# Kernel tuning notes

Measured on AMD Instinct MI355X. Metric: run time of the kernel, lower is better.

## Reference

```python
import jax, jax.numpy as jnp
import numpy as np

MAX_N_LATENT = 8
EOS_THRESHOLD = 0.7
EOS_PATTERN_LEN = 3
COS_SIM_THRESHOLD = 0.3
EOS_SOFT_THRESHOLD = 0.5
CONTEXT_WINDOW = 2
EPS = 1e-8


def setup_inputs() -> dict:
    key = jax.random.key(0)
    k = jax.random.split(key, 8)
    B, S, D = 8, 4096, 1024
    s = 0.02
    latent_states = jax.random.normal(k[0], (B, S, D), dtype=jnp.float32)
    binary_mask = jax.random.randint(k[1], (B, S, 1), 0, 2).astype(jnp.int32)
    proj_w = jax.random.normal(k[2], (D, D), dtype=jnp.float32) * s
    proj_b = jax.random.normal(k[3], (D,), dtype=jnp.float32) * s
    eos_w1 = jax.random.normal(k[4], (D, D // 2), dtype=jnp.float32) * s
    eos_b1 = jax.random.normal(k[5], (D // 2,), dtype=jnp.float32) * s
    eos_w2 = jax.random.normal(k[6], (D // 2, 1), dtype=jnp.float32) * s
    eos_b2 = jax.random.normal(k[7], (1,), dtype=jnp.float32) * s
    return {"latent_states": latent_states, "binary_mask": binary_mask,
            "proj_w": proj_w, "proj_b": proj_b,
            "eos_w1": eos_w1, "eos_b1": eos_b1,
            "eos_w2": eos_w2, "eos_b2": eos_b2}


def reference(latent_states, binary_mask, proj_w, proj_b, eos_w1, eos_b1, eos_w2, eos_b2):
    B, S, D = latent_states.shape

    # ---- EOS scores (computed under no_grad in the original) ----
    h = jax.nn.relu(jnp.einsum('bsd,df->bsf', latent_states, eos_w1) + eos_b1)
    eos_scores = jax.nn.sigmoid(jnp.einsum('bsf,fo->bso', h, eos_w2) + eos_b2)[..., 0]
    eos_scores = jax.lax.stop_gradient(eos_scores)  # [B, S]

    # ---- segment ids: a boundary (mask==1) at i closes the patch that includes i ----
    m = binary_mask[..., 0].astype(jnp.int32)                 # [B, S]
    seg = jnp.cumsum(m, axis=1) - m                           # exclusive cumsum => patch id per token
    valid = (seg < MAX_N_LATENT).astype(latent_states.dtype)  # drop patches beyond MAX_N_LATENT (p[:max_patches])
    onehot = jax.nn.one_hot(jnp.clip(seg, 0, MAX_N_LATENT - 1), MAX_N_LATENT,
                            dtype=latent_states.dtype) * valid[..., None]  # [B, S, P]
    sums = jnp.einsum('bsp,bsd->bpd', onehot, latent_states)  # segmented sum
    counts = onehot.sum(axis=1)                               # [B, P]
    pooled = sums / jnp.maximum(counts, 1.0)[..., None]       # mean pooling; empty patches -> 0 (proj adds bias, as in torch)
    patches = jnp.einsum('bpd,do->bpo', pooled, proj_w) + proj_b  # [B, MAX_N_LATENT, output_dim]

    # ---- EOS bounds ----
    mthr = eos_scores > EOS_THRESHOLD
    run = mthr
    for t in range(1, EOS_PATTERN_LEN):                       # consecutive_eos_count >= EOS_PATTERN_LEN
        run = run & jnp.pad(mthr[:, :-t], ((0, 0), (t, 0)))
    a = latent_states[:, 1:-1]                                # prev state at i-1, for i >= 2
    b = latent_states[:, 2:]                                  # current state at i
    cos = (a * b).sum(-1) / (jnp.maximum(jnp.linalg.norm(a, axis=-1), EPS)
                             * jnp.maximum(jnp.linalg.norm(b, axis=-1), EPS))
    cos_rule = jnp.pad((cos < COS_SIM_THRESHOLD) & (eos_scores[:, 2:] > EOS_SOFT_THRESHOLD),
                       ((0, 0), (2, 0)))
    eos_any = run | cos_rule                                  # [B, S] (duplicate triggers don't change min/max)
    has = eos_any.any()
    idx = jnp.arange(S)[None, :]
    first = jnp.min(jnp.where(eos_any, idx, S))
    last = jnp.max(jnp.where(eos_any, idx, -1))
    start = jnp.maximum(0, first - CONTEXT_WINDOW)
    end = jnp.minimum(S - 1, last + CONTEXT_WINDOW)
    eos_bounds = jnp.where(has, jnp.stack([start, end]), jnp.full((2,), -1))
    return patches, eos_bounds
```

## Files before the change

### kernel.cpp

```cpp
#include <hip/hip_runtime.h>
#include <hip/hip_fp16.h>
#include <cstdint>
#include <cstddef>

#define B_ 8
#define S_ 4096
#define D_ 1024
#define H_ 512
#define M_ (B_*S_)

typedef __attribute__((ext_vector_type(8))) _Float16 half8;
typedef __attribute__((ext_vector_type(16))) float f16v;

union HU { int4 v; half8 h; };

__device__ inline unsigned short f2h(float f){
  _Float16 h = (_Float16)f;
  return __builtin_bit_cast(unsigned short, h);
}

__global__ __launch_bounds__(256) void k_prep(const float* __restrict__ w1,
    unsigned short* __restrict__ w1t, const int* __restrict__ mask,
    int* __restrict__ cb, float* __restrict__ logit, float* __restrict__ gsums,
    float* __restrict__ gcnt, int* __restrict__ fl){
  __shared__ float tile[32][33];
  __shared__ int sc[256];
  int b = blockIdx.x, tid = threadIdx.x;
  if (b < 512){
    int n0 = (b&15)*32, k0 = (b>>4)*32;
    int tx = tid&31, ty = tid>>5;
    #pragma unroll
    for (int i=0;i<4;i++) tile[ty+8*i][tx] = w1[(size_t)(k0+ty+8*i)*H_ + n0+tx];
    __syncthreads();
    #pragma unroll
    for (int i=0;i<4;i++) w1t[(size_t)(n0+ty+8*i)*D_ + k0+tx] = f2h(tile[tx][ty+8*i]);
  } else {
    int bb = b - 512;
    const int* mrow = mask + (size_t)bb*S_ + tid*16;
    int s = 0;
    #pragma unroll
    for (int i=0;i<16;i++) s += mrow[i];
    sc[tid] = s;
    __syncthreads();
    for (int off=1; off<256; off<<=1){
      int v = (tid>=off) ? sc[tid-off] : 0;
      __syncthreads();
      sc[tid] += v;
      __syncthreads();
    }
    if ((tid & 15) == 0) cb[bb*16 + (tid>>4)] = (tid==0) ? 0 : sc[tid-1];
    float4* lz = (float4*)(logit + bb*4096);
    #pragma unroll
    for (int e=tid; e<1024; e+=256) lz[e] = make_float4(0.f,0.f,0.f,0.f);
    float4* gz = (float4*)(gsums + (size_t)bb*8192);
    for (int e=tid; e<2048; e+=256) gz[e] = make_float4(0.f,0.f,0.f,0.f);
    if (bb==0){
      if (tid < 64) gcnt[tid] = 0.f;
      if (tid == 64){ fl[0] = 0x7FFFFFFF; fl[1] = -1; fl[2] = 0; }
    }
  }
}

__global__ void k_normdot(const float* __restrict__ X, float* __restrict__ n2o,
                          float* __restrict__ dto, unsigned short* __restrict__ Xh){
  int wave = threadIdx.x>>6, lane = threadIdx.x&63;
  int g0 = (blockIdx.x*4 + wave)*16;
  const float4* Xv = (const float4*)X;
  ushort4* Xhv = (ushort4*)Xh;
  float4 pv[4];
  if ((g0 & (S_-1)) != 0){
    size_t bb = (size_t)(g0-1)*256;
    #pragma unroll
    for (int q=0;q<4;q++) pv[q] = Xv[bb + q*64 + lane];
  } else {
    #pragma unroll
    for (int q=0;q<4;q++) pv[q] = make_float4(0.f,0.f,0.f,0.f);
  }
  for (int r=0;r<16;r++){
    int g = g0 + r;
    size_t bb = (size_t)g*256;
    float4 cv[4];
    #pragma unroll
    for (int q=0;q<4;q++) cv[q] = Xv[bb + q*64 + lane];
    float n2=0.f, dp=0.f;
    #pragma unroll
    for (int q=0;q<4;q++){
      n2 += cv[q].x*cv[q].x + cv[q].y*cv[q].y + cv[q].z*cv[q].z + cv[q].w*cv[q].w;
      dp += pv[q].x*cv[q].x + pv[q].y*cv[q].y + pv[q].z*cv[q].z + pv[q].w*cv[q].w;
    }
    #pragma unroll
    for (int q=0;q<4;q++){
      ushort4 u;
      u.x = f2h(cv[q].x); u.y = f2h(cv[q].y); u.z = f2h(cv[q].z); u.w = f2h(cv[q].w);
      Xhv[bb + q*64 + lane] = u;
    }
    #pragma unroll
    for (int off=32; off>0; off>>=1){
      n2 += __shfl_down(n2, off);
      dp += __shfl_down(dp, off);
    }
    if (lane==0){
      n2o[g] = n2;
      if ((g & (S_-1)) != 0) dto[g-1] = dp;
    }
    #pragma unroll
    for (int q=0;q<4;q++) pv[q] = cv[q];
  }
}

#define AS1 __attribute__((address_space(1)))
#define AS3 __attribute__((address_space(3)))

__global__ __launch_bounds__(256) void k_mlp(const unsigned short* __restrict__ Xh,
    const unsigned short* __restrict__ W1T, const float* __restrict__ b1,
    const float* __restrict__ w2, float* __restrict__ logit){
  __shared__ __align__(16) unsigned short As[128*64];
  __shared__ __align__(16) unsigned short Bs[128*64];
  int tid = threadIdx.x;
  int wave = tid>>6, lane = tid&63;
  int l31 = lane&31, h = lane>>5;
  int m0 = blockIdx.x*128, n0 = blockIdx.y*128;
  int wm = (wave>>1)*64, wn = (wave&1)*64;
  f16v acc[2][2] = {};

  int arow = lane>>3;
  int cch  = (lane&7) ^ arow;
  const unsigned short* agp[4]; const unsigned short* bgp[4];
  unsigned aldo[4], bldo[4];
  #pragma unroll
  for (int q=0;q<4;q++){
    int rb = wave*32 + q*8;
    agp[q] = Xh  + (size_t)(m0 + rb + arow)*D_ + cch*8;
    bgp[q] = W1T + (size_t)(n0 + rb + arow)*D_ + cch*8;
    aldo[q] = rb*128;
    bldo[q] = rb*128;
  }

  unsigned aoff[2][4], boff[2][4];
  #pragma unroll
  for (int i=0;i<2;i++){
    int m = wm + 32*i + l31;
    int n = wn + 32*i + l31;
    #pragma unroll
    for (int kk=0;kk<4;kk++){
      int c = kk*2 + h;
      aoff[i][kk] = m*128 + (((c ^ (m&7)))<<4);
      boff[i][kk] = n*128 + (((c ^ (n&7)))<<4);
    }
  }

  for (int kt=0; kt<16; ++kt){
    int k0e = kt*64;
    #pragma unroll
    for (int q=0;q<4;q++)
      __builtin_amdgcn_global_load_lds((const AS1 void*)(agp[q] + k0e),
                                       (AS3 void*)((char*)As + aldo[q]), 16, 0, 0);
    #pragma unroll
    for (int q=0;q<4;q++)
      __builtin_amdgcn_global_load_lds((const AS1 void*)(bgp[q] + k0e),
                                       (AS3 void*)((char*)Bs + bldo[q]), 16, 0, 0);
    __syncthreads();
    #pragma unroll
    for (int kk=0;kk<4;kk++){
      HU a0, a1, b0, b1u;
      a0.v  = *(const int4*)((const char*)As + aoff[0][kk]);
      a1.v  = *(const int4*)((const char*)As + aoff[1][kk]);
      b0.v  = *(const int4*)((const char*)Bs + boff[0][kk]);
      b1u.v = *(const int4*)((const char*)Bs + boff[1][kk]);
      acc[0][0] = __builtin_amdgcn_mfma_f32_32x32x16_f16(a0.h, b0.h,  acc[0][0], 0,0,0);
      acc[0][1] = __builtin_amdgcn_mfma_f32_32x32x16_f16(a0.h, b1u.h, acc[0][1], 0,0,0);
      acc[1][0] = __builtin_amdgcn_mfma_f32_32x32x16_f16(a1.h, b0.h,  acc[1][0], 0,0,0);
      acc[1][1] = __builtin_amdgcn_mfma_f32_32x32x16_f16(a1.h, b1u.h, acc[1][1], 0,0,0);
    }
    __syncthreads();
  }

  float b1v[2], w2v[2];
  #pragma unroll
  for (int j=0;j<2;j++){
    int n = n0 + wn + 32*j + l31;
    b1v[j] = b1[n]; w2v[j] = w2[n];
  }
  #pragma unroll
  for (int i=0;i<2;i++){
    #pragma unroll
    for (int r=0;r<16;r++){
      float p = w2v[0]*fmaxf(acc[i][0][r] + b1v[0], 0.f)
              + w2v[1]*fmaxf(acc[i][1][r] + b1v[1], 0.f);
      p += __shfl_xor(p, 1);
      p += __shfl_xor(p, 2);
      p += __shfl_xor(p, 4);
      p += __shfl_xor(p, 8);
      p += __shfl_xor(p, 16);
      if (l31 == 0){
        int row = m0 + wm + 32*i + (r&3) + 8*(r>>2) + 4*h;
        atomicAdd(&logit[row], p);
      }
    }
  }
}

__global__ void k_pool(const float* __restrict__ X, const int* __restrict__ mask,
                       const int* __restrict__ cb, float* __restrict__ gsums,
                       float* __restrict__ gcnt){
  int c = blockIdx.x, b = blockIdx.y, tid = threadIdx.x;
  int base = cb[b*16 + c];
  if (base >= 8) return;
  __shared__ float lsum[8*1024];
  __shared__ int seg[256];
  __shared__ float lcnt[8];
  __shared__ int send_s;
  for (int e=tid; e<8192; e+=256) lsum[e] = 0.f;
  if (tid==0){
    float cnts[8] = {0,0,0,0,0,0,0,0};
    const int* mrow = mask + (size_t)b*S_ + c*256;
    int running = base, i = 0;
    for (; i<256; ++i){
      if (running >= 8) break;
      seg[i] = running;
      cnts[running] += 1.f;
      running += mrow[i];
    }
    send_s = i;
    #pragma unroll
    for (int p=0;p<8;p++) lcnt[p] = cnts[p];
  }
  __syncthreads();
  int send = send_s;
  for (int s2=0; s2<send; ++s2){
    int sg = seg[s2];
    size_t gb = ((size_t)(b*S_ + c*256 + s2))*D_;
    #pragma unroll
    for (int q=0;q<4;q++){
      int d = tid + q*256;
      lsum[sg*1024 + d] += X[gb + d];
    }
  }
  __syncthreads();
  for (int e=tid; e<8192; e+=256){
    float v = lsum[e];
    if (v != 0.f) atomicAdd(&gsums[(size_t)b*8192 + e], v);
  }
  if (tid < 8){
    float v = lcnt[tid];
    if (v != 0.f) atomicAdd(&gcnt[b*8 + tid], v);
  }
}

__global__ __launch_bounds__(256) void k_patch(const float* __restrict__ gsums,
                        const float* __restrict__ gcnt,
                        const float* __restrict__ pw, const float* __restrict__ pb,
                        float* __restrict__ out){
  __shared__ float pool[8192];
  __shared__ float red[2048];
  int b = blockIdx.y, cx = blockIdx.x, tid = threadIdx.x;
  const float4* gs4 = (const float4*)(gsums + (size_t)b*8192);
  float4* pool4 = (float4*)pool;
  for (int e4=tid; e4<2048; e4+=256){
    int p = e4>>8;
    float inv = 1.f / fmaxf(gcnt[b*8 + p], 1.f);
    float4 v = gs4[e4];
    v.x*=inv; v.y*=inv; v.z*=inv; v.w*=inv;
    pool4[e4] = v;
  }
  __syncthreads();
  int c = tid & 31, ks = tid >> 5;
  int col = cx*32 + c;
  float acc[8] = {0,0,0,0,0,0,0,0};
  for (int k=ks*128; k<ks*128+128; ++k){
    float w = pw[(size_t)k*D_ + col];
    #pragma unroll
    for (int p=0;p<8;p++) acc[p] += pool[p*1024 + k]*w;
  }
  #pragma unroll
  for (int p=0;p<8;p++) red[tid*8 + p] = acc[p];
  __syncthreads();
  {
    int p = tid>>5, cc = tid&31;
    float s = 0.f;
    #pragma unroll
    for (int k2=0;k2<8;k2++) s += red[(k2*32 + cc)*8 + p];
    out[(size_t)(b*8+p)*D_ + cx*32 + cc] = s + pb[cx*32 + cc];
  }
}

__global__ void k_flagsb(const float* __restrict__ logit, const float* __restrict__ n2,
                        const float* __restrict__ dt, const float* __restrict__ b2p,
                        int* __restrict__ fl, float* __restrict__ ob){
  int g = blockIdx.x*256 + threadIdx.x;
  float b2 = b2p[0];
  int s = g & (S_-1);
  bool any = false;
  if (s >= 2){
    float z0 = logit[g] + b2;
    float z1 = logit[g-1] + b2;
    float z2 = logit[g-2] + b2;
    const float THR = 0.8472978603872037f;
    bool run = (z0 > THR) & (z1 > THR) & (z2 > THR);
    float na = fmaxf(sqrtf(n2[g-1]), 1e-8f);
    float nb = fmaxf(sqrtf(n2[g]), 1e-8f);
    bool cosr = (dt[g-1] < 0.3f*na*nb) & (z0 > 0.f);
    any = run | cosr;
  }
  int mn = any ? s : 0x7FFFFFFF;
  int mx = any ? s : -1;
  #pragma unroll
  for (int off=32; off>0; off>>=1){
    mn = min(mn, __shfl_down(mn, off));
    mx = max(mx, __shfl_down(mx, off));
  }
  if ((threadIdx.x & 63) == 0){
    atomicMin(&fl[0], mn);
    atomicMax(&fl[1], mx);
  }
  __syncthreads();
  if (threadIdx.x == 0){
    __threadfence();
    int old = atomicAdd(&fl[2], 1);
    if (old == gridDim.x - 1){
      int f = atomicMin(&fl[0], 0x7FFFFFFF);
      int l = atomicMax(&fl[1], (int)0x80000000);
      if (l < 0){ ob[0] = -1.f; ob[1] = -1.f; }
      else {
        int st = f - 2; if (st < 0) st = 0;
        int en = l + 2; if (en > S_-1) en = S_-1;
        ob[0] = (float)st; ob[1] = (float)en;
      }
    }
  }
}

extern "C" void kernel_launch(void* const* d_in, const int* in_sizes, int n_in,
                              void* d_out, int out_size, void* d_ws, size_t ws_size,
                              hipStream_t stream){
  const float* latent = (const float*)d_in[0];
  const int*   mask   = (const int*)d_in[1];
  const float* proj_w = (const float*)d_in[2];
  const float* proj_b = (const float*)d_in[3];
  const float* eos_w1 = (const float*)d_in[4];
  const float* eos_b1 = (const float*)d_in[5];
  const float* eos_w2 = (const float*)d_in[6];
  const float* eos_b2 = (const float*)d_in[7];
  float* out = (float*)d_out;

  char* ws = (char*)d_ws;
  unsigned short* W1T = (unsigned short*)ws;
  unsigned short* Xh  = (unsigned short*)(ws + 1048576);
  float* fbase = (float*)(ws + 1048576 + 67108864);
  float* logit = fbase;
  float* norm2 = fbase + 32768;
  float* dotv  = fbase + 65536;
  float* gsums = fbase + 98304;
  float* gcnt  = fbase + 163840;
  int* chunkbase = (int*)(fbase + 163904);
  int* fl        = (int*)(fbase + 164032);

  k_prep<<<520, 256, 0, stream>>>(eos_w1, W1T, mask, chunkbase, logit, gsums, gcnt, fl);
  k_normdot<<<512, 256, 0, stream>>>(latent, norm2, dotv, Xh);
  k_pool<<<dim3(16,8), 256, 0, stream>>>(latent, mask, chunkbase, gsums, gcnt);
  k_patch<<<dim3(32,8), 256, 0, stream>>>(gsums, gcnt, proj_w, proj_b, out);
  k_mlp<<<dim3(256,4), 256, 0, stream>>>(Xh, W1T, eos_b1, eos_w2, logit);
  k_flagsb<<<128, 256, 0, stream>>>(logit, norm2, dotv, eos_b2, fl, out + 65536);
}
```

Baseline: 317.5 us.

## Double-buffer MLP GEMM LDS tiles and merge prep with norm/convert kernel

The k_mlp GEMM now uses a two-stage LDS ring with 32-wide K tiles, so the next tile is issued before the current one is consumed and one barrier per iteration is removed. The swizzle is reworked for the narrower tile. The grid is flattened so the four N-tiles of one M block are adjacent, which helps L2 reuse of the A rows. The norm/dot/fp16-convert kernel is merged into the prep kernel to save a launch and let the two run concurrently. The risk is less work per barrier from the smaller K tile.

```diff
diff --git a/kernel.cpp b/kernel.cpp
--- a/kernel.cpp
+++ b/kernel.cpp
@@ -19,14 +19,60 @@
   return __builtin_bit_cast(unsigned short, h);
 }
 
-__global__ __launch_bounds__(256) void k_prep(const float* __restrict__ w1,
-    unsigned short* __restrict__ w1t, const int* __restrict__ mask,
-    int* __restrict__ cb, float* __restrict__ logit, float* __restrict__ gsums,
-    float* __restrict__ gcnt, int* __restrict__ fl){
+__global__ __launch_bounds__(256) void k_pre(const float* __restrict__ X,
+    float* __restrict__ n2o, float* __restrict__ dto, unsigned short* __restrict__ Xh,
+    const float* __restrict__ w1, unsigned short* __restrict__ w1t,
+    const int* __restrict__ mask, int* __restrict__ cb, float* __restrict__ logit,
+    float* __restrict__ gsums, float* __restrict__ gcnt, int* __restrict__ fl){
   __shared__ float tile[32][33];
   __shared__ int sc[256];
-  int b = blockIdx.x, tid = threadIdx.x;
-  if (b < 512){
+  int bid = blockIdx.x, tid = threadIdx.x;
+  if (bid < 512){
+    int wave = tid>>6, lane = tid&63;
+    int g0 = (bid*4 + wave)*16;
+    const float4* Xv = (const float4*)X;
+    ushort4* Xhv = (ushort4*)Xh;
+    float4 pv[4];
+    if ((g0 & (S_-1)) != 0){
+      size_t bb = (size_t)(g0-1)*256;
+      #pragma unroll
+      for (int q=0;q<4;q++) pv[q] = Xv[bb + q*64 + lane];
+    } else {
+      #pragma unroll
+      for (int q=0;q<4;q++) pv[q] = make_float4(0.f,0.f,0.f,0.f);
+    }
+    for (int r=0;r<16;r++){
+      int g = g0 + r;
+      size_t bb = (size_t)g*256;
+      float4 cv[4];
+      #pragma unroll
+      for (int q=0;q<4;q++) cv[q] = Xv[bb + q*64 + lane];
+      float n2=0.f, dp=0.f;
+      #pragma unroll
+      for (int q=0;q<4;q++){
+        n2 += cv[q].x*cv[q].x + cv[q].y*cv[q].y + cv[q].z*cv[q].z + cv[q].w*cv[q].w;
+        dp += pv[q].x*cv[q].x + pv[q].y*cv[q].y + pv[q].z*cv[q].z + pv[q].w*cv[q].w;
+      }
+      #pragma unroll
+      for (int q=0;q<4;q++){
+        ushort4 u;
+        u.x = f2h(cv[q].x); u.y = f2h(cv[q].y); u.z = f2h(cv[q].z); u.w = f2h(cv[q].w);
+        Xhv[bb + q*64 + lane] = u;
+      }
+      #pragma unroll
+      for (int off=32; off>0; off>>=1){
+        n2 += __shfl_down(n2, off);
+        dp += __shfl_down(dp, off);
+      }
+      if (lane==0){
+        n2o[g] = n2;
+        if ((g & (S_-1)) != 0) dto[g-1] = dp;
+      }
+      #pragma unroll
+      for (int q=0;q<4;q++) pv[q] = cv[q];
+    }
+  } else if (bid < 1024){
+    int b = bid - 512;
     int n0 = (b&15)*32, k0 = (b>>4)*32;
     int tx = tid&31, ty = tid>>5;
     #pragma unroll
@@ -35,7 +81,7 @@
     #pragma unroll
     for (int i=0;i<4;i++) w1t[(size_t)(n0+ty+8*i)*D_ + k0+tx] = f2h(tile[tx][ty+8*i]);
   } else {
-    int bb = b - 512;
+    int bb = bid - 1024;
     const int* mrow = mask + (size_t)bb*S_ + tid*16;
     int s = 0;
     #pragma unroll
@@ -61,126 +107,82 @@
   }
 }
 
-__global__ void k_normdot(const float* __restrict__ X, float* __restrict__ n2o,
-                          float* __restrict__ dto, unsigned short* __restrict__ Xh){
-  int wave = threadIdx.x>>6, lane = threadIdx.x&63;
-  int g0 = (blockIdx.x*4 + wave)*16;
-  const float4* Xv = (const float4*)X;
-  ushort4* Xhv = (ushort4*)Xh;
-  float4 pv[4];
-  if ((g0 & (S_-1)) != 0){
-    size_t bb = (size_t)(g0-1)*256;
-    #pragma unroll
-    for (int q=0;q<4;q++) pv[q] = Xv[bb + q*64 + lane];
-  } else {
-    #pragma unroll
-    for (int q=0;q<4;q++) pv[q] = make_float4(0.f,0.f,0.f,0.f);
-  }
-  for (int r=0;r<16;r++){
-    int g = g0 + r;
-    size_t bb = (size_t)g*256;
-    float4 cv[4];
-    #pragma unroll
-    for (int q=0;q<4;q++) cv[q] = Xv[bb + q*64 + lane];
-    float n2=0.f, dp=0.f;
-    #pragma unroll
-    for (int q=0;q<4;q++){
-      n2 += cv[q].x*cv[q].x + cv[q].y*cv[q].y + cv[q].z*cv[q].z + cv[q].w*cv[q].w;
-      dp += pv[q].x*cv[q].x + pv[q].y*cv[q].y + pv[q].z*cv[q].z + pv[q].w*cv[q].w;
-    }
-    #pragma unroll
-    for (int q=0;q<4;q++){
-      ushort4 u;
-      u.x = f2h(cv[q].x); u.y = f2h(cv[q].y); u.z = f2h(cv[q].z); u.w = f2h(cv[q].w);
-      Xhv[bb + q*64 + lane] = u;
-    }
-    #pragma unroll
-    for (int off=32; off>0; off>>=1){
-      n2 += __shfl_down(n2, off);
-      dp += __shfl_down(dp, off);
-    }
-    if (lane==0){
-      n2o[g] = n2;
-      if ((g & (S_-1)) != 0) dto[g-1] = dp;
-    }
-    #pragma unroll
-    for (int q=0;q<4;q++) pv[q] = cv[q];
-  }
-}
-
 #define AS1 __attribute__((address_space(1)))
 #define AS3 __attribute__((address_space(3)))
+
+#define STAGE(kt_, nb_) do { int k0e = (kt_)*32; \
+  char* abase = (char*)As[nb_]; char* bbase = (char*)Bs[nb_]; \
+  _Pragma("unroll") for (int q=0;q<2;q++){ \
+    __builtin_amdgcn_global_load_lds((const AS1 void*)(agp[q]+k0e), (AS3 void*)(abase+aldo[q]),16,0,0); \
+    __builtin_amdgcn_global_load_lds((const AS1 void*)(bgp[q]+k0e), (AS3 void*)(bbase+bldo[q]),16,0,0); } \
+} while(0)
 
 __global__ __launch_bounds__(256) void k_mlp(const unsigned short* __restrict__ Xh,
     const unsigned short* __restrict__ W1T, const float* __restrict__ b1,
     const float* __restrict__ w2, float* __restrict__ logit){
-  __shared__ __align__(16) unsigned short As[128*64];
-  __shared__ __align__(16) unsigned short Bs[128*64];
+  __shared__ __align__(16) unsigned short As[2][128*32];
+  __shared__ __align__(16) unsigned short Bs[2][128*32];
   int tid = threadIdx.x;
   int wave = tid>>6, lane = tid&63;
   int l31 = lane&31, h = lane>>5;
-  int m0 = blockIdx.x*128, n0 = blockIdx.y*128;
+  int m0 = (blockIdx.x>>2)*128, n0 = (blockIdx.x&3)*128;
   int wm = (wave>>1)*64, wn = (wave&1)*64;
   f16v acc[2][2] = {};
 
-  int arow = lane>>3;
-  int cch  = (lane&7) ^ arow;
-  const unsigned short* agp[4]; const unsigned short* bgp[4];
-  unsigned aldo[4], bldo[4];
-  #pragma unroll
-  for (int q=0;q<4;q++){
-    int rb = wave*32 + q*8;
-    agp[q] = Xh  + (size_t)(m0 + rb + arow)*D_ + cch*8;
-    bgp[q] = W1T + (size_t)(n0 + rb + arow)*D_ + cch*8;
-    aldo[q] = rb*128;
-    bldo[q] = rb*128;
-  }
-
-  unsigned aoff[2][4], boff[2][4];
+  int srow = lane>>2;
+  const unsigned short* agp[2]; const unsigned short* bgp[2];
+  unsigned aldo[2], bldo[2];
+  #pragma unroll
+  for (int q=0;q<2;q++){
+    int rb = wave*32 + q*16;
+    int r  = rb + srow;
+    int c  = (lane&3) ^ ((r>>1)&3);
+    agp[q] = Xh  + (size_t)(m0 + r)*D_ + c*8;
+    bgp[q] = W1T + (size_t)(n0 + r)*D_ + c*8;
+    aldo[q] = rb*64;
+    bldo[q] = rb*64;
+  }
+
+  unsigned aoff[2][2], boff[2][2];
   #pragma unroll
   for (int i=0;i<2;i++){
-    int m = wm + 32*i + l31;
-    int n = wn + 32*i + l31;
-    #pragma unroll
-    for (int kk=0;kk<4;kk++){
+    int rm = wm + 32*i + l31;
+    int rn = wn + 32*i + l31;
+    #pragma unroll
+    for (int kk=0;kk<2;kk++){
       int c = kk*2 + h;
-      aoff[i][kk] = m*128 + (((c ^ (m&7)))<<4);
-      boff[i][kk] = n*128 + (((c ^ (n&7)))<<4);
-    }
-  }
-
-  for (int kt=0; kt<16; ++kt){
-    int k0e = kt*64;
-    #pragma unroll
-    for (int q=0;q<4;q++)
-      __builtin_amdgcn_global_load_lds((const AS1 void*)(agp[q] + k0e),
-                                       (AS3 void*)((char*)As + aldo[q]), 16, 0, 0);
-    #pragma unroll
-    for (int q=0;q<4;q++)
-      __builtin_amdgcn_global_load_lds((const AS1 void*)(bgp[q] + k0e),
-                                       (AS3 void*)((char*)Bs + bldo[q]), 16, 0, 0);
+      aoff[i][kk] = rm*64 + ((c ^ ((rm>>1)&3))<<4);
+      boff[i][kk] = rn*64 + ((c ^ ((rn>>1)&3))<<4);
+    }
+  }
+
+  float b1v[2], w2v[2];
+  #pragma unroll
+  for (int j=0;j<2;j++){
+    int n = n0 + wn + 32*j + l31;
+    b1v[j] = b1[n]; w2v[j] = w2[n];
+  }
+
+  STAGE(0, 0);
+  for (int kt=0; kt<32; ++kt){
     __syncthreads();
-    #pragma unroll
-    for (int kk=0;kk<4;kk++){
+    if (kt < 31) STAGE(kt+1, (kt+1)&1);
+    const char* ab = (const char*)As[kt&1];
+    const char* bb = (const char*)Bs[kt&1];
+    #pragma unroll
+    for (int kk=0;kk<2;kk++){
       HU a0, a1, b0, b1u;
-      a0.v  = *(const int4*)((const char*)As + aoff[0][kk]);
-      a1.v  = *(const int4*)((const char*)As + aoff[1][kk]);
-      b0.v  = *(const int4*)((const char*)Bs + boff[0][kk]);
-      b1u.v = *(const int4*)((const char*)Bs + boff[1][kk]);
+      a0.v  = *(const int4*)(ab + aoff[0][kk]);
+      a1.v  = *(const int4*)(ab + aoff[1][kk]);
+      b0.v  = *(const int4*)(bb + boff[0][kk]);
+      b1u.v = *(const int4*)(bb + boff[1][kk]);
       acc[0][0] = __builtin_amdgcn_mfma_f32_32x32x16_f16(a0.h, b0.h,  acc[0][0], 0,0,0);
       acc[0][1] = __builtin_amdgcn_mfma_f32_32x32x16_f16(a0.h, b1u.h, acc[0][1], 0,0,0);
       acc[1][0] = __builtin_amdgcn_mfma_f32_32x32x16_f16(a1.h, b0.h,  acc[1][0], 0,0,0);
       acc[1][1] = __builtin_amdgcn_mfma_f32_32x32x16_f16(a1.h, b1u.h, acc[1][1], 0,0,0);
     }
-    __syncthreads();
-  }
-
-  float b1v[2], w2v[2];
-  #pragma unroll
-  for (int j=0;j<2;j++){
-    int n = n0 + wn + 32*j + l31;
-    b1v[j] = b1[n]; w2v[j] = w2[n];
-  }
+  }
+
   #pragma unroll
   for (int i=0;i<2;i++){
     #pragma unroll
@@ -355,10 +357,10 @@
   int* chunkbase = (int*)(fbase + 163904);
   int* fl        = (int*)(fbase + 164032);
 
-  k_prep<<<520, 256, 0, stream>>>(eos_w1, W1T, mask, chunkbase, logit, gsums, gcnt, fl);
-  k_normdot<<<512, 256, 0, stream>>>(latent, norm2, dotv, Xh);
+  k_pre<<<1032, 256, 0, stream>>>(latent, norm2, dotv, Xh, eos_w1, W1T, mask,
+                                  chunkbase, logit, gsums, gcnt, fl);
   k_pool<<<dim3(16,8), 256, 0, stream>>>(latent, mask, chunkbase, gsums, gcnt);
   k_patch<<<dim3(32,8), 256, 0, stream>>>(gsums, gcnt, proj_w, proj_b, out);
-  k_mlp<<<dim3(256,4), 256, 0, stream>>>(Xh, W1T, eos_b1, eos_w2, logit);
+  k_mlp<<<1024, 256, 0, stream>>>(Xh, W1T, eos_b1, eos_w2, logit);
   k_flagsb<<<128, 256, 0, stream>>>(logit, norm2, dotv, eos_b2, fl, out + 65536);
 }
```

Result: no change. 314.5 us (-0.9%).
